# Kernel tuning notes

Measured on AMD Instinct MI355X. Metric: run time of the kernel, lower is better.

Reference implementation:

```python
import jax, jax.numpy as jnp
import numpy as np

B, S, D_IN, D_OUT = 4, 4096, 2048, 2048


def setup_inputs() -> dict:
    key = jax.random.key(0)
    kx, kw = jax.random.split(key)
    x = jax.random.normal(kx, (B, S, D_IN), dtype=jnp.float32)
    weight = jax.random.normal(kw, (D_OUT, D_IN), dtype=jnp.float32) * 0.02
    return {"x": x, "weight": weight}


def reference(x, weight):
    # Per-row absmax int8 activation quantization
    x_scale = jnp.clip(jnp.max(jnp.abs(x), axis=-1, keepdims=True), 1e-05, None)  # [B,S,1]
    x_quant = jnp.clip(jnp.round(x / x_scale * 127.0), -128.0, 127.0)
    # Ternary weight quantization (mean-centered absmean scale)
    w_mean = jnp.mean(weight)
    w_centered = weight - w_mean
    w_scale = jnp.clip(jnp.mean(jnp.abs(w_centered)), 1e-05, None)
    w_quant = jnp.clip(jnp.round(w_centered / w_scale), -1.0, 1.0)
    # GEMM on quantized values, then dequant rescale
    y = jnp.einsum('bsi,oi->bso', x_quant, w_quant)  # [B,S,D_OUT]
    y = y * (w_scale * x_scale / 127.0)
    return y.astype(x.dtype)
```

## Files before the change

kernel.cpp:

```cpp
#include <hip/hip_runtime.h>
#include <stdint.h>

#define M_TOT 16384
#define K_DIM 2048
#define N_DIM 2048
#define W_ELEMS (N_DIM * K_DIM)

typedef int v4i  __attribute__((ext_vector_type(4)));
typedef int v16i __attribute__((ext_vector_type(16)));

__device__ __forceinline__ void async_load16(const void* gptr, void* lptr) {
    __builtin_amdgcn_global_load_lds(
        (__attribute__((address_space(1))) void*)(uintptr_t)gptr,
        (__attribute__((address_space(3))) void*)(uint32_t)(uintptr_t)lptr,
        16, 0, 0);
}

__device__ __forceinline__ int qclamp(float v, int lo, int hi) {
    int q = (int)rintf(v);
    q = q > hi ? hi : (q < lo ? lo : q);
    return q & 255;
}

__global__ __launch_bounds__(256) void wsum_kernel(const float* __restrict__ w,
                                                   double* __restrict__ spart) {
    int tid = blockIdx.x * 256 + threadIdx.x;
    const float4* w4 = (const float4*)w;
    double s = 0.0;
    #pragma unroll
    for (int it = 0; it < 8; it++) {
        float4 v = w4[tid + it * 131072];
        s += (double)v.x + (double)v.y + (double)v.z + (double)v.w;
    }
    #pragma unroll
    for (int off = 32; off; off >>= 1) s += __shfl_down(s, off);
    __shared__ double ls[4];
    if ((threadIdx.x & 63) == 0) ls[threadIdx.x >> 6] = s;
    __syncthreads();
    if (threadIdx.x == 0) spart[blockIdx.x] = ls[0] + ls[1] + ls[2] + ls[3];
}

__global__ __launch_bounds__(256) void wabs_kernel(const float* __restrict__ w,
                                                   const double* __restrict__ spart,
                                                   double* __restrict__ apart) {
    __shared__ double ls[4];
    double sm = spart[threadIdx.x] + spart[threadIdx.x + 256];
    #pragma unroll
    for (int off = 32; off; off >>= 1) sm += __shfl_down(sm, off);
    if ((threadIdx.x & 63) == 0) ls[threadIdx.x >> 6] = sm;
    __syncthreads();
    double mean = (ls[0] + ls[1] + ls[2] + ls[3]) * (1.0 / (double)W_ELEMS);
    __syncthreads();
    int tid = blockIdx.x * 256 + threadIdx.x;
    const float4* w4 = (const float4*)w;
    double s = 0.0;
    #pragma unroll
    for (int it = 0; it < 8; it++) {
        float4 v = w4[tid + it * 131072];
        s += fabs((double)v.x - mean) + fabs((double)v.y - mean) +
             fabs((double)v.z - mean) + fabs((double)v.w - mean);
    }
    #pragma unroll
    for (int off = 32; off; off >>= 1) s += __shfl_down(s, off);
    if ((threadIdx.x & 63) == 0) ls[threadIdx.x >> 6] = s;
    __syncthreads();
    if (threadIdx.x == 0) apart[blockIdx.x] = ls[0] + ls[1] + ls[2] + ls[3];
}

__global__ __launch_bounds__(256) void quant_kernel(
    const float* __restrict__ x, const float* __restrict__ w,
    const double* __restrict__ spart, const double* __restrict__ apart,
    int8_t* __restrict__ xq, int8_t* __restrict__ wq,
    float* __restrict__ xscale, float* __restrict__ wsf)
{
    const int t = threadIdx.x;
    if (blockIdx.x < 4096) {
        const int row  = (blockIdx.x << 2) | (t >> 6);
        const int lane = t & 63;
        const float4* xr = (const float4*)(x + (size_t)row * K_DIM);
        float4 v[8];
        #pragma unroll
        for (int i = 0; i < 8; i++) v[i] = xr[lane + (i << 6)];
        float m = 0.0f;
        #pragma unroll
        for (int i = 0; i < 8; i++)
            m = fmaxf(m, fmaxf(fmaxf(fabsf(v[i].x), fabsf(v[i].y)),
                               fmaxf(fabsf(v[i].z), fabsf(v[i].w))));
        #pragma unroll
        for (int off = 32; off; off >>= 1) m = fmaxf(m, __shfl_xor(m, off));
        const float scale = fmaxf(m, 1e-5f);
        if (lane == 0) xscale[row] = scale;
        int* outp = (int*)(xq + (size_t)row * K_DIM);
        #pragma unroll
        for (int i = 0; i < 8; i++) {
            int p = qclamp(v[i].x / scale * 127.0f, -128, 127)
                  | (qclamp(v[i].y / scale * 127.0f, -128, 127) << 8)
                  | (qclamp(v[i].z / scale * 127.0f, -128, 127) << 16)
                  | (qclamp(v[i].w / scale * 127.0f, -128, 127) << 24);
            outp[lane + (i << 6)] = p;
        }
    } else {
        __shared__ double ls0[4], ls1[4];
        double s0 = spart[t] + spart[t + 256];
        double s1 = apart[t] + apart[t + 256];
        #pragma unroll
        for (int off = 32; off; off >>= 1) {
            s0 += __shfl_down(s0, off);
            s1 += __shfl_down(s1, off);
        }
        if ((t & 63) == 0) { ls0[t >> 6] = s0; ls1[t >> 6] = s1; }
        __syncthreads();
        float mean  = (float)((ls0[0] + ls0[1] + ls0[2] + ls0[3]) * (1.0 / (double)W_ELEMS));
        float scale = (float)fmax((ls1[0] + ls1[1] + ls1[2] + ls1[3]) * (1.0 / (double)W_ELEMS), 1e-5);
        int i = (blockIdx.x - 4096) * 256 + t;
        float4 v = ((const float4*)w)[i];
        int p = qclamp((v.x - mean) / scale, -1, 1)
              | (qclamp((v.y - mean) / scale, -1, 1) << 8)
              | (qclamp((v.z - mean) / scale, -1, 1) << 16)
              | (qclamp((v.w - mean) / scale, -1, 1) << 24);
        ((int*)wq)[i] = p;
        if (i == 0) wsf[0] = scale * (1.0f / 127.0f);
    }
}

__global__ __launch_bounds__(512, 2) void gemm_i8_kernel(
    const int8_t* __restrict__ xq, const int8_t* __restrict__ wq,
    const float* __restrict__ xscale, const float* __restrict__ wsf,
    float* __restrict__ out)
{
    __shared__ __align__(16) int8_t lsA[2][32768];
    __shared__ __align__(16) int8_t lsB[2][32768];

    const int tid  = threadIdx.x;
    const int lane = tid & 63;
    const int wv   = tid >> 6;

    const int flat = blockIdx.x;
    const int nf   = ((flat & 7) << 6) | (flat >> 3);
    const int bm   = nf >> 3;
    const int bn   = nf & 7;

    const int sChunk = (((tid & 7) ^ ((tid >> 3) & 7)) << 4);
    const int8_t* gAb = xq + (size_t)(bm * 256 + (tid >> 3)) * K_DIM + sChunk;
    const int8_t* gBb = wq + (size_t)(bn * 256 + (tid >> 3)) * K_DIM + sChunk;
    const int sDst = tid * 16;

    #define STAGE(NB, K0)                                                      \
        do {                                                                   \
            _Pragma("unroll")                                                  \
            for (int g_ = 0; g_ < 4; g_++)                                     \
                async_load16(gAb + (size_t)g_ * 64 * K_DIM + (K0),             \
                             lsA[NB] + g_ * 8192 + sDst);                      \
            _Pragma("unroll")                                                  \
            for (int g_ = 0; g_ < 4; g_++)                                     \
                async_load16(gBb + (size_t)g_ * 64 * K_DIM + (K0),             \
                             lsB[NB] + g_ * 8192 + sDst);                      \
        } while (0)

    const int wm  = (wv >> 2) << 7;
    const int wn  = (wv & 3) << 6;
    const int l31 = lane & 31;
    const int hi  = lane >> 5;
    const int lx  = lane & 7;

    int rA[4], rB[2], cs[4];
    #pragma unroll
    for (int mi = 0; mi < 4; mi++) rA[mi] = (wm + mi * 32 + l31) << 7;
    #pragma unroll
    for (int nj = 0; nj < 2; nj++) rB[nj] = (wn + nj * 32 + l31) << 7;
    #pragma unroll
    for (int ks = 0; ks < 4; ks++) cs[ks] = ((ks * 2 + hi) ^ lx) << 4;

    v16i acc[4][2] = {};

    STAGE(0, 0);
    asm volatile("s_waitcnt vmcnt(0)" ::: "memory");
    __builtin_amdgcn_s_barrier();

    for (int t = 0; t < 16; ++t) {
        const int cur = t & 1;
        const int8_t* pA = lsA[cur];
        const int8_t* pB = lsB[cur];
        if (t < 15) STAGE(cur ^ 1, (t + 1) << 7);
        __builtin_amdgcn_s_setprio(1);
        #pragma unroll
        for (int ks = 0; ks < 4; ks++) {
            v4i af[4], bf[2];
            #pragma unroll
            for (int mi = 0; mi < 4; mi++)
                af[mi] = *(const v4i*)(pA + rA[mi] + cs[ks]);
            #pragma unroll
            for (int nj = 0; nj < 2; nj++)
                bf[nj] = *(const v4i*)(pB + rB[nj] + cs[ks]);
            #pragma unroll
            for (int mi = 0; mi < 4; mi++)
                #pragma unroll
                for (int nj = 0; nj < 2; nj++)
                    acc[mi][nj] = __builtin_amdgcn_mfma_i32_32x32x32_i8(
                        af[mi], bf[nj], acc[mi][nj], 0, 0, 0);
        }
        __builtin_amdgcn_s_setprio(0);
        asm volatile("s_waitcnt vmcnt(0) lgkmcnt(0)" ::: "memory");
        __builtin_amdgcn_s_barrier();
    }
    #undef STAGE

    const float f127 = wsf[0];
    #pragma unroll
    for (int mi = 0; mi < 4; mi++) {
        #pragma unroll
        for (int r = 0; r < 16; r++) {
            const int rowl = (r & 3) + ((r >> 2) << 3) + (hi << 2);
            const int mg = bm * 256 + wm + mi * 32 + rowl;
            const float fs = f127 * xscale[mg];
            float* orow = out + (size_t)mg * N_DIM + bn * 256 + wn + l31;
            #pragma unroll
            for (int nj = 0; nj < 2; nj++)
                orow[nj * 32] = fs * (float)acc[mi][nj][r];
        }
    }
}

extern "C" void kernel_launch(void* const* d_in, const int* in_sizes, int n_in,
                              void* d_out, int out_size, void* d_ws, size_t ws_size,
                              hipStream_t stream) {
    const float* x = (const float*)d_in[0];
    const float* w = (const float*)d_in[1];
    float* out = (float*)d_out;

    char* ws = (char*)d_ws;
    double* spart  = (double*)ws;
    double* apart  = (double*)(ws + 4096);
    float*  wsf    = (float*)(ws + 8192);
    float*  xscale = (float*)(ws + 12288);
    int8_t* xq     = (int8_t*)(ws + 12288 + 65536);
    int8_t* wq     = xq + (size_t)M_TOT * K_DIM;

    wsum_kernel <<<512, 256, 0, stream>>>(w, spart);
    wabs_kernel <<<512, 256, 0, stream>>>(w, spart, apart);
    quant_kernel<<<8192, 256, 0, stream>>>(x, w, spart, apart, xq, wq, xscale, wsf);
    gemm_i8_kernel<<<512, 512, 0, stream>>>(xq, wq, xscale, wsf, out);
}
```

Before: 312.3 us.

## Pre-tile ternary weights for direct register loads and drop B LDS staging

The weight quantizer now writes int8 weights in an MFMA-fragment-friendly tiled layout, so each wave can load its B operand fragments straight from global memory into registers. B's shared-memory double buffer goes away and B is register double-buffered across K tiles. The A staging changes to a new LDS layout and swizzle. The aim is to cut LDS traffic and shared-memory footprint for B. The cost is that B fragments loaded redundantly per wave now go through global/L2, and more registers are used for prefetched fragments.

```diff
diff --git a/kernel.cpp b/kernel.cpp
--- a/kernel.cpp
+++ b/kernel.cpp
@@ -118,7 +118,9 @@
               | (qclamp((v.y - mean) / scale, -1, 1) << 8)
               | (qclamp((v.z - mean) / scale, -1, 1) << 16)
               | (qclamp((v.w - mean) / scale, -1, 1) << 24);
-        ((int*)wq)[i] = p;
+        const int o  = i >> 9;
+        const int kw = i & 511;
+        ((int*)wq)[((o >> 5) << 14) + ((kw >> 2) << 7) + ((o & 31) << 2) + (kw & 3)] = p;
         if (i == 0) wsf[0] = scale * (1.0f / 127.0f);
     }
 }
@@ -129,7 +131,6 @@
     float* __restrict__ out)
 {
     __shared__ __align__(16) int8_t lsA[2][32768];
-    __shared__ __align__(16) int8_t lsB[2][32768];
 
     const int tid  = threadIdx.x;
     const int lane = tid & 63;
@@ -140,72 +141,86 @@
     const int bm   = nf >> 3;
     const int bn   = nf & 7;
 
-    const int sChunk = (((tid & 7) ^ ((tid >> 3) & 7)) << 4);
-    const int8_t* gAb = xq + (size_t)(bm * 256 + (tid >> 3)) * K_DIM + sChunk;
-    const int8_t* gBb = wq + (size_t)(bn * 256 + (tid >> 3)) * K_DIM + sChunk;
-    const int sDst = tid * 16;
-
-    #define STAGE(NB, K0)                                                      \
+    const int sChunkA = (((tid & 3) ^ ((tid >> 3) & 3)) << 4);
+    const int8_t* gAb = xq + (size_t)(bm * 256 + (tid >> 2)) * K_DIM + sChunkA;
+
+    #define STAGE_A(NB, K0)                                                    \
+        do {                                                                   \
+            async_load16(gAb + (K0),                      lsA[NB] + tid * 16); \
+            async_load16(gAb + (K0) + (size_t)128 * K_DIM,                     \
+                         lsA[NB] + 8192 + tid * 16);                           \
+            async_load16(gAb + (K0) + 64,                 lsA[NB] + 16384 + tid * 16); \
+            async_load16(gAb + (K0) + 64 + (size_t)128 * K_DIM,                \
+                         lsA[NB] + 16384 + 8192 + tid * 16);                   \
+        } while (0)
+
+    const int wm  = (wv >> 2) << 7;
+    const int l31 = lane & 31;
+    const int hi  = lane >> 5;
+    const int rx  = (l31 >> 1) & 3;
+
+    int abase[4];
+    #pragma unroll
+    for (int mi = 0; mi < 4; mi++) abase[mi] = (wm + mi * 32 + l31) << 6;
+    int kslot[4];
+    #pragma unroll
+    for (int ks = 0; ks < 4; ks++)
+        kslot[ks] = ((ks >> 1) << 14) + (((((ks & 1) << 1) | hi) ^ rx) << 4);
+
+    const int rb0 = bn * 8 + (wv & 3) * 2;
+    const int8_t* gB0 = wq + ((size_t)rb0 << 16) + (hi << 9) + (l31 << 4);
+    const int8_t* gB1 = gB0 + 65536;
+
+    v4i bfA[2][4], bfB[2][4];
+    #define LOADB(DST, T)                                                      \
         do {                                                                   \
             _Pragma("unroll")                                                  \
-            for (int g_ = 0; g_ < 4; g_++)                                     \
-                async_load16(gAb + (size_t)g_ * 64 * K_DIM + (K0),             \
-                             lsA[NB] + g_ * 8192 + sDst);                      \
+            for (int ks_ = 0; ks_ < 4; ks_++) {                                \
+                DST[0][ks_] = *(const v4i*)(gB0 + (T) * 4096 + ks_ * 1024);    \
+                DST[1][ks_] = *(const v4i*)(gB1 + (T) * 4096 + ks_ * 1024);    \
+            }                                                                  \
+        } while (0)
+
+    v16i acc[4][2] = {};
+
+    #define TILE(CUR, NXT, T, CB, NB)                                          \
+        do {                                                                   \
+            if ((T) < 15) { STAGE_A(NB, ((T) + 1) << 7); LOADB(NXT, (T) + 1); }\
+            const int8_t* pA_ = lsA[CB];                                       \
+            __builtin_amdgcn_s_setprio(1);                                     \
             _Pragma("unroll")                                                  \
-            for (int g_ = 0; g_ < 4; g_++)                                     \
-                async_load16(gBb + (size_t)g_ * 64 * K_DIM + (K0),             \
-                             lsB[NB] + g_ * 8192 + sDst);                      \
+            for (int ks_ = 0; ks_ < 4; ks_++) {                                \
+                v4i af[4];                                                     \
+                _Pragma("unroll")                                              \
+                for (int mi_ = 0; mi_ < 4; mi_++)                              \
+                    af[mi_] = *(const v4i*)(pA_ + abase[mi_] + kslot[ks_]);    \
+                _Pragma("unroll")                                              \
+                for (int mi_ = 0; mi_ < 4; mi_++)                              \
+                    _Pragma("unroll")                                          \
+                    for (int nj_ = 0; nj_ < 2; nj_++)                          \
+                        acc[mi_][nj_] = __builtin_amdgcn_mfma_i32_32x32x32_i8( \
+                            af[mi_], CUR[nj_][ks_], acc[mi_][nj_], 0, 0, 0);   \
+            }                                                                  \
+            __builtin_amdgcn_s_setprio(0);                                     \
+            asm volatile("s_waitcnt vmcnt(0) lgkmcnt(0)" ::: "memory");        \
+            __builtin_amdgcn_s_barrier();                                      \
         } while (0)
 
-    const int wm  = (wv >> 2) << 7;
-    const int wn  = (wv & 3) << 6;
-    const int l31 = lane & 31;
-    const int hi  = lane >> 5;
-    const int lx  = lane & 7;
-
-    int rA[4], rB[2], cs[4];
-    #pragma unroll
-    for (int mi = 0; mi < 4; mi++) rA[mi] = (wm + mi * 32 + l31) << 7;
-    #pragma unroll
-    for (int nj = 0; nj < 2; nj++) rB[nj] = (wn + nj * 32 + l31) << 7;
-    #pragma unroll
-    for (int ks = 0; ks < 4; ks++) cs[ks] = ((ks * 2 + hi) ^ lx) << 4;
-
-    v16i acc[4][2] = {};
-
-    STAGE(0, 0);
+    STAGE_A(0, 0);
+    LOADB(bfA, 0);
     asm volatile("s_waitcnt vmcnt(0)" ::: "memory");
     __builtin_amdgcn_s_barrier();
 
-    for (int t = 0; t < 16; ++t) {
-        const int cur = t & 1;
-        const int8_t* pA = lsA[cur];
-        const int8_t* pB = lsB[cur];
-        if (t < 15) STAGE(cur ^ 1, (t + 1) << 7);
-        __builtin_amdgcn_s_setprio(1);
-        #pragma unroll
-        for (int ks = 0; ks < 4; ks++) {
-            v4i af[4], bf[2];
-            #pragma unroll
-            for (int mi = 0; mi < 4; mi++)
-                af[mi] = *(const v4i*)(pA + rA[mi] + cs[ks]);
-            #pragma unroll
-            for (int nj = 0; nj < 2; nj++)
-                bf[nj] = *(const v4i*)(pB + rB[nj] + cs[ks]);
-            #pragma unroll
-            for (int mi = 0; mi < 4; mi++)
-                #pragma unroll
-                for (int nj = 0; nj < 2; nj++)
-                    acc[mi][nj] = __builtin_amdgcn_mfma_i32_32x32x32_i8(
-                        af[mi], bf[nj], acc[mi][nj], 0, 0, 0);
-        }
-        __builtin_amdgcn_s_setprio(0);
-        asm volatile("s_waitcnt vmcnt(0) lgkmcnt(0)" ::: "memory");
-        __builtin_amdgcn_s_barrier();
-    }
-    #undef STAGE
+    for (int tt = 0; tt < 16; tt += 2) {
+        TILE(bfA, bfB, tt,     0, 1);
+        TILE(bfB, bfA, tt + 1, 1, 0);
+    }
+    #undef TILE
+    #undef LOADB
+    #undef STAGE_A
 
     const float f127 = wsf[0];
+    const int wn = (wv & 3) << 6;
     #pragma unroll
     for (int mi = 0; mi < 4; mi++) {
         #pragma unroll
```

After: 318.8 us. +2.1%, slower.

## Switch GEMM to 16x16x64 i8 MFMA with 64-wide K tiles

Applied to the files above, without the earlier changes.

Replaces the 32x32x32 int8 MFMA tiling with 16x16x64 MFMA fragments (8x4 per wave), halves the K-step per stage to 64 so LDS buffers shrink to 16KB each, and adds a matching XOR swizzle for the new row width. The main loop is unrolled in pairs with compile-time buffer indices, and the epilogue is rewritten for the 16x16 output layout. The intent is to lower LDS use (room for more occupancy), simplify addressing, and use a possibly higher-throughput MFMA shape. In exchange there are twice as many barriers and global-to-LDS stages, each covering less work.

```diff
diff --git a/kernel.cpp b/kernel.cpp
--- a/kernel.cpp
+++ b/kernel.cpp
@@ -7,7 +7,6 @@
 #define W_ELEMS (N_DIM * K_DIM)
 
 typedef int v4i  __attribute__((ext_vector_type(4)));
-typedef int v16i __attribute__((ext_vector_type(16)));
 
 __device__ __forceinline__ void async_load16(const void* gptr, void* lptr) {
     __builtin_amdgcn_global_load_lds(
@@ -128,8 +127,8 @@
     const float* __restrict__ xscale, const float* __restrict__ wsf,
     float* __restrict__ out)
 {
-    __shared__ __align__(16) int8_t lsA[2][32768];
-    __shared__ __align__(16) int8_t lsB[2][32768];
+    __shared__ __align__(16) int8_t lsA[2][16384];
+    __shared__ __align__(16) int8_t lsB[2][16384];
 
     const int tid  = threadIdx.x;
     const int lane = tid & 63;
@@ -140,83 +139,80 @@
     const int bm   = nf >> 3;
     const int bn   = nf & 7;
 
-    const int sChunk = (((tid & 7) ^ ((tid >> 3) & 7)) << 4);
-    const int8_t* gAb = xq + (size_t)(bm * 256 + (tid >> 3)) * K_DIM + sChunk;
-    const int8_t* gBb = wq + (size_t)(bn * 256 + (tid >> 3)) * K_DIM + sChunk;
-    const int sDst = tid * 16;
+    const int sChunk = (((tid & 3) ^ ((tid >> 3) & 3)) << 4);
+    const int8_t* gAb = xq + (size_t)(bm * 256 + (tid >> 2)) * K_DIM + sChunk;
+    const int8_t* gBb = wq + (size_t)(bn * 256 + (tid >> 2)) * K_DIM + sChunk;
 
     #define STAGE(NB, K0)                                                      \
         do {                                                                   \
+            async_load16(gAb + (K0),                       lsA[NB] + tid * 16);\
+            async_load16(gAb + (K0) + (size_t)128 * K_DIM, lsA[NB] + 8192 + tid * 16); \
+            async_load16(gBb + (K0),                       lsB[NB] + tid * 16);\
+            async_load16(gBb + (K0) + (size_t)128 * K_DIM, lsB[NB] + 8192 + tid * 16); \
+        } while (0)
+
+    const int wm = (wv >> 2) << 7;
+    const int wn = (wv & 3) << 6;
+    const int fr = lane & 15;
+    const int fc = lane >> 4;
+    int aoff[8], boff[4];
+    #pragma unroll
+    for (int mi = 0; mi < 8; mi++) {
+        int ra = wm + mi * 16 + fr;
+        aoff[mi] = ra * 64 + ((fc ^ ((ra >> 1) & 3)) << 4);
+    }
+    #pragma unroll
+    for (int nj = 0; nj < 4; nj++) {
+        int rb = wn + nj * 16 + fr;
+        boff[nj] = rb * 64 + ((fc ^ ((rb >> 1) & 3)) << 4);
+    }
+
+    v4i acc[8][4] = {};
+
+    #define TILE(CB, T)                                                        \
+        do {                                                                   \
+            if ((T) < 31) STAGE((CB) ^ 1, ((T) + 1) << 6);                     \
+            v4i af[8], bf[4];                                                  \
             _Pragma("unroll")                                                  \
-            for (int g_ = 0; g_ < 4; g_++)                                     \
-                async_load16(gAb + (size_t)g_ * 64 * K_DIM + (K0),             \
-                             lsA[NB] + g_ * 8192 + sDst);                      \
+            for (int mi_ = 0; mi_ < 8; mi_++)                                  \
+                af[mi_] = *(const v4i*)(lsA[CB] + aoff[mi_]);                  \
             _Pragma("unroll")                                                  \
-            for (int g_ = 0; g_ < 4; g_++)                                     \
-                async_load16(gBb + (size_t)g_ * 64 * K_DIM + (K0),             \
-                             lsB[NB] + g_ * 8192 + sDst);                      \
+            for (int nj_ = 0; nj_ < 4; nj_++)                                  \
+                bf[nj_] = *(const v4i*)(lsB[CB] + boff[nj_]);                  \
+            __builtin_amdgcn_s_setprio(1);                                     \
+            _Pragma("unroll")                                                  \
+            for (int mi_ = 0; mi_ < 8; mi_++)                                  \
+                _Pragma("unroll")                                              \
+                for (int nj_ = 0; nj_ < 4; nj_++)                              \
+                    acc[mi_][nj_] = __builtin_amdgcn_mfma_i32_16x16x64_i8(     \
+                        af[mi_], bf[nj_], acc[mi_][nj_], 0, 0, 0);             \
+            __builtin_amdgcn_s_setprio(0);                                     \
+            asm volatile("s_waitcnt vmcnt(0) lgkmcnt(0)" ::: "memory");        \
+            __builtin_amdgcn_s_barrier();                                      \
         } while (0)
-
-    const int wm  = (wv >> 2) << 7;
-    const int wn  = (wv & 3) << 6;
-    const int l31 = lane & 31;
-    const int hi  = lane >> 5;
-    const int lx  = lane & 7;
-
-    int rA[4], rB[2], cs[4];
-    #pragma unroll
-    for (int mi = 0; mi < 4; mi++) rA[mi] = (wm + mi * 32 + l31) << 7;
-    #pragma unroll
-    for (int nj = 0; nj < 2; nj++) rB[nj] = (wn + nj * 32 + l31) << 7;
-    #pragma unroll
-    for (int ks = 0; ks < 4; ks++) cs[ks] = ((ks * 2 + hi) ^ lx) << 4;
-
-    v16i acc[4][2] = {};
 
     STAGE(0, 0);
     asm volatile("s_waitcnt vmcnt(0)" ::: "memory");
     __builtin_amdgcn_s_barrier();
 
-    for (int t = 0; t < 16; ++t) {
-        const int cur = t & 1;
-        const int8_t* pA = lsA[cur];
-        const int8_t* pB = lsB[cur];
-        if (t < 15) STAGE(cur ^ 1, (t + 1) << 7);
-        __builtin_amdgcn_s_setprio(1);
-        #pragma unroll
-        for (int ks = 0; ks < 4; ks++) {
-            v4i af[4], bf[2];
+    for (int t = 0; t < 32; t += 2) {
+        TILE(0, t);
+        TILE(1, t + 1);
+    }
+    #undef TILE
+    #undef STAGE
+
+    const float f127 = wsf[0];
+    #pragma unroll
+    for (int mi = 0; mi < 8; mi++) {
+        #pragma unroll
+        for (int rg = 0; rg < 4; rg++) {
+            const int mg = bm * 256 + wm + mi * 16 + (lane >> 4) * 4 + rg;
+            const float fs = f127 * xscale[mg];
+            float* orow = out + (size_t)mg * N_DIM + bn * 256 + wn;
             #pragma unroll
-            for (int mi = 0; mi < 4; mi++)
-                af[mi] = *(const v4i*)(pA + rA[mi] + cs[ks]);
-            #pragma unroll
-            for (int nj = 0; nj < 2; nj++)
-                bf[nj] = *(const v4i*)(pB + rB[nj] + cs[ks]);
-            #pragma unroll
-            for (int mi = 0; mi < 4; mi++)
-                #pragma unroll
-                for (int nj = 0; nj < 2; nj++)
-                    acc[mi][nj] = __builtin_amdgcn_mfma_i32_32x32x32_i8(
-                        af[mi], bf[nj], acc[mi][nj], 0, 0, 0);
-        }
-        __builtin_amdgcn_s_setprio(0);
-        asm volatile("s_waitcnt vmcnt(0) lgkmcnt(0)" ::: "memory");
-        __builtin_amdgcn_s_barrier();
-    }
-    #undef STAGE
-
-    const float f127 = wsf[0];
-    #pragma unroll
-    for (int mi = 0; mi < 4; mi++) {
-        #pragma unroll
-        for (int r = 0; r < 16; r++) {
-            const int rowl = (r & 3) + ((r >> 2) << 3) + (hi << 2);
-            const int mg = bm * 256 + wm + mi * 32 + rowl;
-            const float fs = f127 * xscale[mg];
-            float* orow = out + (size_t)mg * N_DIM + bn * 256 + wn + l31;
-            #pragma unroll
-            for (int nj = 0; nj < 2; nj++)
-                orow[nj * 32] = fs * (float)acc[mi][nj][r];
+            for (int nj = 0; nj < 4; nj++)
+                orow[nj * 16 + fr] = fs * (float)acc[mi][nj][rg];
         }
     }
 }
```

Measured after the change: 308.8 us. Within noise of the previous version (-1.1%).
